# Optimization experiments

Hardware: AMD Instinct MI355X
Metric: run time of the kernel (lower is better)

The kernel has to match this reference:

```python
import jax, jax.numpy as jnp
import numpy as np

DT = 1e-11
DX = 0.01
EPS0 = 8.854e-12
MU0 = 4 * 3.1415926 * 1e-07
C_EPS = DT / EPS0 / DX  # dt_eps / dx
C_MU = DT / MU0 / DX    # dt_mu / dx

B, NX, NY = 2, 4096, 4096


def setup_inputs() -> dict:
    key = jax.random.key(0)
    k1, k2, k3 = jax.random.split(key, 3)
    shape = (B, 1, NX, NY)
    return {
        "Ez": jax.random.normal(k1, shape, dtype=jnp.float32),
        "Hx": jax.random.normal(k2, shape, dtype=jnp.float32),
        "Hy": jax.random.normal(k3, shape, dtype=jnp.float32),
    }


def reference(Ez, Hx, Hy):
    c_mu = jnp.float32(C_MU)
    c_eps = jnp.float32(C_EPS)
    # H updates (use old Ez)
    Hx = Hx.at[:, :, :-1, :].add(-c_mu * (Ez[:, :, 1:, :] - Ez[:, :, :-1, :]))
    Hy = Hy.at[:, :, :, :-1].add(c_mu * (Ez[:, :, :, 1:] - Ez[:, :, :, :-1]))
    # Ez update uses the NEW Hx/Hy (matches in-place torch semantics)
    curl = (Hy[:, :, 1:, 1:] - Hy[:, :, :-1, 1:]) - (Hx[:, :, 1:, 1:] - Hx[:, :, 1:, :-1])
    Ez = Ez.at[:, :, 1:, 1:].add(c_eps * curl)
    return (Ez, Hx, Hy)
```

## Files before the change

kernel.cpp:

```cpp
#include <hip/hip_runtime.h>

#define NXd 4096
#define NYd 4096
#define Bd  2

constexpr double DTd   = 1e-11;
constexpr double DXd   = 0.01;
constexpr double EPS0d = 8.854e-12;
constexpr double MU0d  = 4.0 * 3.1415926 * 1e-07;
constexpr float  C_EPS = (float)(DTd / EPS0d / DXd);
constexpr float  C_MU  = (float)(DTd / MU0d / DXd);

__global__ __launch_bounds__(256) void fdtd_step_kernel(
    const float* __restrict__ Ez, const float* __restrict__ Hx,
    const float* __restrict__ Hy,
    float* __restrict__ EzO, float* __restrict__ HxO, float* __restrict__ HyO)
{
    const int j0 = (blockIdx.x * 256 + threadIdx.x) * 4;
    const int i  = blockIdx.y;
    const int b  = blockIdx.z;
    const size_t base = ((size_t)b * NXd + (size_t)i) * NYd + j0;
    const float* ez = Ez + base;

    const bool has_down = (i < NXd - 1);
    const bool has_up   = (i > 0);
    const bool jm_ok    = (j0 > 0);
    const bool jp_ok    = (j0 + 4 < NYd);

    float4 ec = *(const float4*)(ez);
    float ezc0 = jm_ok ? ez[-1] : 0.f;
    float ezc5 = jp_ok ? ez[4]  : 0.f;

    float4 ed = make_float4(0.f, 0.f, 0.f, 0.f);
    float ezd0 = 0.f;
    if (has_down) {
        ed = *(const float4*)(ez + NYd);
        ezd0 = jm_ok ? ez[NYd - 1] : 0.f;
    }

    float4 eu  = make_float4(0.f, 0.f, 0.f, 0.f);
    float ezu4 = 0.f;
    float4 hyu = make_float4(0.f, 0.f, 0.f, 0.f);
    if (has_up) {
        eu   = *(const float4*)(ez - NYd);
        ezu4 = jp_ok ? ez[-NYd + 4] : 0.f;
        hyu  = *(const float4*)(Hy + base - NYd);
    }

    float4 hxc  = *(const float4*)(Hx + base);
    float  hxm1 = jm_ok ? Hx[base - 1] : 0.f;
    float4 hyc  = *(const float4*)(Hy + base);

    float ezc[6] = {ezc0, ec.x, ec.y, ec.z, ec.w, ezc5};
    float ezd[5] = {ezd0, ed.x, ed.y, ed.z, ed.w};
    float ezu[5] = {eu.x, eu.y, eu.z, eu.w, ezu4};
    float hx_[5] = {hxm1, hxc.x, hxc.y, hxc.z, hxc.w};
    float hy_[4] = {hyc.x, hyc.y, hyc.z, hyc.w};
    float hyu_[4]= {hyu.x, hyu.y, hyu.z, hyu.w};

    float hxn[5];
#pragma unroll
    for (int t = 0; t < 5; ++t)
        hxn[t] = has_down ? fmaf(-C_MU, ezd[t] - ezc[t], hx_[t]) : hx_[t];

    float hyn[4], hyun[4];
#pragma unroll
    for (int k = 0; k < 4; ++k) {
        const bool jn = (j0 + k) < (NYd - 1);
        hyn[k]  = jn ? fmaf(C_MU, ezc[k + 2] - ezc[k + 1], hy_[k])  : hy_[k];
        hyun[k] = jn ? fmaf(C_MU, ezu[k + 1] - ezu[k],     hyu_[k]) : hyu_[k];
    }

    float ezn[4];
#pragma unroll
    for (int k = 0; k < 4; ++k) {
        const bool upd = has_up && ((j0 + k) >= 1);
        const float curl = (hyn[k] - hyun[k]) - (hxn[k + 1] - hxn[k]);
        ezn[k] = upd ? fmaf(C_EPS, curl, ezc[k + 1]) : ezc[k + 1];
    }

    *(float4*)(EzO + base) = make_float4(ezn[0], ezn[1], ezn[2], ezn[3]);
    *(float4*)(HxO + base) = make_float4(hxn[1], hxn[2], hxn[3], hxn[4]);
    *(float4*)(HyO + base) = make_float4(hyn[0], hyn[1], hyn[2], hyn[3]);
}

extern "C" void kernel_launch(void* const* d_in, const int* in_sizes, int n_in,
                              void* d_out, int out_size, void* d_ws, size_t ws_size,
                              hipStream_t stream) {
    const float* Ez = (const float*)d_in[0];
    const float* Hx = (const float*)d_in[1];
    const float* Hy = (const float*)d_in[2];
    float* out = (float*)d_out;
    const size_t N = (size_t)Bd * NXd * NYd;

    dim3 grid(NYd / (256 * 4), NXd, Bd);
    fdtd_step_kernel<<<grid, dim3(256, 1, 1), 0, stream>>>(
        Ez, Hx, Hy, out, out + N, out + 2 * N);
}
```

Measured before the change: 641.1 us.

## Stream multiple rows per thread and reuse Ez and Hy rows in registers

Each thread now walks down 16 consecutive rows, carrying the current and next Ez rows and the previous row's updated Hy in registers. This removes the redundant loads of the up and down Ez rows and the recomputation of the upper Hy row. The grid shrinks by 16x in the row dimension, which lowers parallelism and may reduce latency hiding for a memory-bound kernel.

```diff
diff --git a/kernel.cpp b/kernel.cpp
--- a/kernel.cpp
+++ b/kernel.cpp
@@ -3,6 +3,7 @@
 #define NXd 4096
 #define NYd 4096
 #define Bd  2
+#define RROWS 16
 
 constexpr double DTd   = 1e-11;
 constexpr double DXd   = 0.01;
@@ -11,77 +12,93 @@
 constexpr float  C_EPS = (float)(DTd / EPS0d / DXd);
 constexpr float  C_MU  = (float)(DTd / MU0d / DXd);
 
+__device__ __forceinline__ void load_row6(const float* __restrict__ p, size_t idx,
+                                          bool jm_ok, bool jp_ok, float e[6]) {
+    float4 v = *(const float4*)(p + idx);
+    e[0] = jm_ok ? p[idx - 1] : 0.f;
+    e[1] = v.x; e[2] = v.y; e[3] = v.z; e[4] = v.w;
+    e[5] = jp_ok ? p[idx + 4] : 0.f;
+}
+
 __global__ __launch_bounds__(256) void fdtd_step_kernel(
     const float* __restrict__ Ez, const float* __restrict__ Hx,
     const float* __restrict__ Hy,
     float* __restrict__ EzO, float* __restrict__ HxO, float* __restrict__ HyO)
 {
     const int j0 = (blockIdx.x * 256 + threadIdx.x) * 4;
-    const int i  = blockIdx.y;
+    const int r0 = blockIdx.y * RROWS;
     const int b  = blockIdx.z;
-    const size_t base = ((size_t)b * NXd + (size_t)i) * NYd + j0;
-    const float* ez = Ez + base;
 
-    const bool has_down = (i < NXd - 1);
-    const bool has_up   = (i > 0);
-    const bool jm_ok    = (j0 > 0);
-    const bool jp_ok    = (j0 + 4 < NYd);
+    const bool jm_ok = (j0 > 0);
+    const bool jp_ok = (j0 + 4 < NYd);
 
-    float4 ec = *(const float4*)(ez);
-    float ezc0 = jm_ok ? ez[-1] : 0.f;
-    float ezc5 = jp_ok ? ez[4]  : 0.f;
+    const size_t plane = (size_t)b * NXd * NYd + j0;
 
-    float4 ed = make_float4(0.f, 0.f, 0.f, 0.f);
-    float ezd0 = 0.f;
-    if (has_down) {
-        ed = *(const float4*)(ez + NYd);
-        ezd0 = jm_ok ? ez[NYd - 1] : 0.f;
+    float ez_c[6], ez_m[6], hynm[4];
+    load_row6(Ez, plane + (size_t)r0 * NYd, jm_ok, jp_ok, ez_c);
+    if (r0 > 0) {
+        const size_t bm = plane + (size_t)(r0 - 1) * NYd;
+        load_row6(Ez, bm, jm_ok, jp_ok, ez_m);
+        float4 hym = *(const float4*)(Hy + bm);
+        float hymv[4] = {hym.x, hym.y, hym.z, hym.w};
+#pragma unroll
+        for (int k = 0; k < 4; ++k) {
+            const bool jn = (j0 + k) < (NYd - 1);
+            hynm[k] = jn ? fmaf(C_MU, ez_m[k + 2] - ez_m[k + 1], hymv[k]) : hymv[k];
+        }
+    } else {
+#pragma unroll
+        for (int k = 0; k < 4; ++k) hynm[k] = 0.f;
     }
 
-    float4 eu  = make_float4(0.f, 0.f, 0.f, 0.f);
-    float ezu4 = 0.f;
-    float4 hyu = make_float4(0.f, 0.f, 0.f, 0.f);
-    if (has_up) {
-        eu   = *(const float4*)(ez - NYd);
-        ezu4 = jp_ok ? ez[-NYd + 4] : 0.f;
-        hyu  = *(const float4*)(Hy + base - NYd);
+    for (int i = r0; i < r0 + RROWS; ++i) {
+        const size_t base = plane + (size_t)i * NYd;
+        const bool has_down = (i < NXd - 1);
+        const bool has_up   = (i > 0);
+
+        float ez_p[6];
+        if (has_down) {
+            load_row6(Ez, base + NYd, jm_ok, jp_ok, ez_p);
+        } else {
+#pragma unroll
+            for (int t = 0; t < 6; ++t) ez_p[t] = 0.f;
+        }
+
+        float4 hxc = *(const float4*)(Hx + base);
+        float  hxm1 = jm_ok ? Hx[base - 1] : 0.f;
+        float4 hyc = *(const float4*)(Hy + base);
+        float hx_[5] = {hxm1, hxc.x, hxc.y, hxc.z, hxc.w};
+        float hy_[4] = {hyc.x, hyc.y, hyc.z, hyc.w};
+
+        float hxn[5];
+#pragma unroll
+        for (int t = 0; t < 5; ++t)
+            hxn[t] = has_down ? fmaf(-C_MU, ez_p[t] - ez_c[t], hx_[t]) : hx_[t];
+
+        float hyn[4];
+#pragma unroll
+        for (int k = 0; k < 4; ++k) {
+            const bool jn = (j0 + k) < (NYd - 1);
+            hyn[k] = jn ? fmaf(C_MU, ez_c[k + 2] - ez_c[k + 1], hy_[k]) : hy_[k];
+        }
+
+        float ezn[4];
+#pragma unroll
+        for (int k = 0; k < 4; ++k) {
+            const bool upd = has_up && ((j0 + k) >= 1);
+            const float curl = (hyn[k] - hynm[k]) - (hxn[k + 1] - hxn[k]);
+            ezn[k] = upd ? fmaf(C_EPS, curl, ez_c[k + 1]) : ez_c[k + 1];
+        }
+
+        *(float4*)(EzO + base) = make_float4(ezn[0], ezn[1], ezn[2], ezn[3]);
+        *(float4*)(HxO + base) = make_float4(hxn[1], hxn[2], hxn[3], hxn[4]);
+        *(float4*)(HyO + base) = make_float4(hyn[0], hyn[1], hyn[2], hyn[3]);
+
+#pragma unroll
+        for (int t = 0; t < 6; ++t) { ez_m[t] = ez_c[t]; ez_c[t] = ez_p[t]; }
+#pragma unroll
+        for (int k = 0; k < 4; ++k) hynm[k] = hyn[k];
     }
-
-    float4 hxc  = *(const float4*)(Hx + base);
-    float  hxm1 = jm_ok ? Hx[base - 1] : 0.f;
-    float4 hyc  = *(const float4*)(Hy + base);
-
-    float ezc[6] = {ezc0, ec.x, ec.y, ec.z, ec.w, ezc5};
-    float ezd[5] = {ezd0, ed.x, ed.y, ed.z, ed.w};
-    float ezu[5] = {eu.x, eu.y, eu.z, eu.w, ezu4};
-    float hx_[5] = {hxm1, hxc.x, hxc.y, hxc.z, hxc.w};
-    float hy_[4] = {hyc.x, hyc.y, hyc.z, hyc.w};
-    float hyu_[4]= {hyu.x, hyu.y, hyu.z, hyu.w};
-
-    float hxn[5];
-#pragma unroll
-    for (int t = 0; t < 5; ++t)
-        hxn[t] = has_down ? fmaf(-C_MU, ezd[t] - ezc[t], hx_[t]) : hx_[t];
-
-    float hyn[4], hyun[4];
-#pragma unroll
-    for (int k = 0; k < 4; ++k) {
-        const bool jn = (j0 + k) < (NYd - 1);
-        hyn[k]  = jn ? fmaf(C_MU, ezc[k + 2] - ezc[k + 1], hy_[k])  : hy_[k];
-        hyun[k] = jn ? fmaf(C_MU, ezu[k + 1] - ezu[k],     hyu_[k]) : hyu_[k];
-    }
-
-    float ezn[4];
-#pragma unroll
-    for (int k = 0; k < 4; ++k) {
-        const bool upd = has_up && ((j0 + k) >= 1);
-        const float curl = (hyn[k] - hyun[k]) - (hxn[k + 1] - hxn[k]);
-        ezn[k] = upd ? fmaf(C_EPS, curl, ezc[k + 1]) : ezc[k + 1];
-    }
-
-    *(float4*)(EzO + base) = make_float4(ezn[0], ezn[1], ezn[2], ezn[3]);
-    *(float4*)(HxO + base) = make_float4(hxn[1], hxn[2], hxn[3], hxn[4]);
-    *(float4*)(HyO + base) = make_float4(hyn[0], hyn[1], hyn[2], hyn[3]);
 }
 
 extern "C" void kernel_launch(void* const* d_in, const int* in_sizes, int n_in,
@@ -93,7 +110,7 @@
     float* out = (float*)d_out;
     const size_t N = (size_t)Bd * NXd * NYd;
 
-    dim3 grid(NYd / (256 * 4), NXd, Bd);
+    dim3 grid(NYd / (256 * 4), NXd / RROWS, Bd);
     fdtd_step_kernel<<<grid, dim3(256, 1, 1), 0, stream>>>(
         Ez, Hx, Hy, out, out + N, out + 2 * N);
 }
```

New measurement: 652.9 us. Within noise of the previous version (+1.8%).
